# Kernel optimization log

Hardware: AMD Instinct MI355X
Metric: run time of the kernel (lower is better)

The kernel has to match this reference:

```python
import jax, jax.numpy as jnp
import numpy as np

N_STATE = 1024
N_HEAD = 16
HEAD_DIM = N_STATE // N_HEAD


def setup_inputs() -> dict:
    key = jax.random.key(0)
    ks = jax.random.split(key, 8)
    B, S = 8, 1500
    x = jax.random.normal(ks[0], (B, S, N_STATE), dtype=jnp.float32)
    # additive causal mask (0 on/below diagonal, -inf above), broadcast over B,H
    neg = jnp.float32(-1e9)
    mask = jnp.where(jnp.tril(jnp.ones((S, S), dtype=bool)), 0.0, neg).astype(jnp.float32)
    s = 0.02
    Wq = jax.random.normal(ks[1], (N_STATE, N_STATE), dtype=jnp.float32) * s
    bq = jnp.zeros((N_STATE,), dtype=jnp.float32)
    Wk = jax.random.normal(ks[2], (N_STATE, N_STATE), dtype=jnp.float32) * s
    Wv = jax.random.normal(ks[3], (N_STATE, N_STATE), dtype=jnp.float32) * s
    bv = jnp.zeros((N_STATE,), dtype=jnp.float32)
    Wo = jax.random.normal(ks[4], (N_STATE, N_STATE), dtype=jnp.float32) * s
    bo = jnp.zeros((N_STATE,), dtype=jnp.float32)
    return {"x": x, "mask": mask, "Wq": Wq, "bq": bq, "Wk": Wk, "Wv": Wv, "bv": bv, "Wo": Wo, "bo": bo}


def reference(x, mask, Wq, bq, Wk, Wv, bv, Wo, bo):
    B, S, _ = x.shape
    # linear projections (torch Linear: x @ W^T + b); W stored as [out, in]
    q = x @ Wq.T + bq
    k = x @ Wk.T
    v = x @ Wv.T + bv
    # [B, H, S, D]
    q = q.reshape(B, S, N_HEAD, HEAD_DIM).transpose(0, 2, 1, 3)
    k = k.reshape(B, S, N_HEAD, HEAD_DIM).transpose(0, 2, 1, 3)
    v = v.reshape(B, S, N_HEAD, HEAD_DIM).transpose(0, 2, 1, 3)
    scale = 1.0 / np.sqrt(HEAD_DIM).astype(np.float32)
    scores = jnp.einsum('bhqd,bhkd->bhqk', q, k) * scale + mask
    attn = jax.nn.softmax(scores, axis=-1)
    out = jnp.einsum('bhqk,bhkd->bhqd', attn, v)
    out = out.transpose(0, 2, 1, 3).reshape(B, S, N_STATE)
    return out @ Wo.T + bo
```

## Files before the change

kernel.cpp:

```cpp
#include <hip/hip_runtime.h>
#include <hip/hip_bf16.h>

#define N_STATE 1024
#define N_HEAD  16
#define D_HEAD  64
#define BATCH   8
#define SEQ     1500
#define ROWS    (BATCH*SEQ)
#define SVP     1536
#define MTILES  94

#define BM 128
#define BN 128
#define BK 32
#define BK2 64

typedef __bf16 bf16x8 __attribute__((ext_vector_type(8)));
typedef __bf16 bf16x4 __attribute__((ext_vector_type(4)));
typedef float  f32x4  __attribute__((ext_vector_type(4)));

__device__ __forceinline__ f32x4 mfma16(bf16x8 a, bf16x8 b, f32x4 c) {
  return __builtin_amdgcn_mfma_f32_16x16x32_bf16(a, b, c, 0, 0, 0);
}

__device__ __forceinline__ void gl_lds16(const void* g, void* l) {
  __builtin_amdgcn_global_load_lds(
      (const __attribute__((address_space(1))) unsigned int*)g,
      (__attribute__((address_space(3))) unsigned int*)l, 16, 0, 0);
}

__global__ __launch_bounds__(256)
void cvt_all(const float* __restrict__ x,  const float* __restrict__ wq,
             const float* __restrict__ wk, const float* __restrict__ wv,
             const float* __restrict__ wo,
             __bf16* __restrict__ xb, __bf16* __restrict__ wb)
{
  const int which = blockIdx.y;
  const float* src;
  __bf16* dst;
  size_t n;
  if (which == 0) { src = x; dst = xb; n = (size_t)ROWS * N_STATE; }
  else {
    src = (which == 1) ? wq : (which == 2) ? wk : (which == 3) ? wv : wo;
    dst = wb + (size_t)(which - 1) * N_STATE * N_STATE;
    n = (size_t)N_STATE * N_STATE;
  }
  const size_t stride = (size_t)gridDim.x * 256 * 4;
  for (size_t i = ((size_t)blockIdx.x * 256 + threadIdx.x) * 4; i < n; i += stride) {
    const f32x4 v = *(const f32x4*)(src + i);
    bf16x4 c; c[0]=(__bf16)v[0]; c[1]=(__bf16)v[1]; c[2]=(__bf16)v[2]; c[3]=(__bf16)v[3];
    *(bf16x4*)(dst + i) = c;
  }
}

__global__ __launch_bounds__(256)
void qkv_fast(const __bf16* __restrict__ xb, const __bf16* __restrict__ wb,
              const float* __restrict__ bq, const float* __restrict__ bv,
              __bf16* __restrict__ q_ws, __bf16* __restrict__ k_ws,
              __bf16* __restrict__ vt_ws)
{
  const int xcd = blockIdx.x & 7;
  const int jj  = blockIdx.x >> 3;
  const int nt  = jj & 7;
  const int mt  = (jj >> 3) * 8 + xcd;
  if (mt >= MTILES) return;

  __shared__ __bf16 lA[BM * BK2];
  __shared__ __bf16 lB[BN * BK2];
  const int which = blockIdx.z;
  const __bf16* W = wb + (size_t)which * N_STATE * N_STATE;

  const int tid = threadIdx.x;
  const int lane = tid & 63, wave = tid >> 6;
  const int l15 = lane & 15, quad = lane >> 4;
  const int wr = wave >> 1, wc = wave & 1;

  f32x4 acc[4][4] = {};

  for (int k0 = 0; k0 < N_STATE; k0 += BK2) {
#pragma unroll
    for (int t = 0; t < 4; ++t) {
      const int c = wave * 4 + t;
      const int s = c * 64 + lane;
      const int row = s >> 3;
      const int sw  = (lane & 7) ^ (row & 7);
      const int ga = min(mt * BM + row, ROWS - 1);
      gl_lds16(xb + (size_t)ga * N_STATE + k0 + sw * 8, (__bf16*)lA + c * 512);
      const int gb = nt * BN + row;
      gl_lds16(W + (size_t)gb * N_STATE + k0 + sw * 8, (__bf16*)lB + c * 512);
    }
    __syncthreads();
#pragma unroll
    for (int h = 0; h < 2; ++h) {
      bf16x8 af[4], bfr[4];
#pragma unroll
      for (int i = 0; i < 4; ++i) {
        const int ra = wr * 64 + i * 16 + l15;
        const int rb = wc * 64 + i * 16 + l15;
        af[i]  = *(const bf16x8*)&lA[ra * BK2 + (((h * 4 + quad) ^ (ra & 7)) * 8)];
        bfr[i] = *(const bf16x8*)&lB[rb * BK2 + (((h * 4 + quad) ^ (rb & 7)) * 8)];
      }
      if (which != 2) {
#pragma unroll
        for (int i = 0; i < 4; ++i)
#pragma unroll
          for (int j = 0; j < 4; ++j)
            acc[i][j] = mfma16(af[i], bfr[j], acc[i][j]);
      } else {
#pragma unroll
        for (int i = 0; i < 4; ++i)
#pragma unroll
          for (int j = 0; j < 4; ++j)
            acc[i][j] = mfma16(bfr[j], af[i], acc[i][j]);
      }
    }
    __syncthreads();
  }

  if (which != 2) {
#pragma unroll
    for (int i = 0; i < 4; ++i) {
      const int mrow = mt * BM + wr * 64 + i * 16 + quad * 4;
#pragma unroll
      for (int j = 0; j < 4; ++j) {
        const int col = nt * BN + wc * 64 + j * 16 + l15;
        const int h = col >> 6, d = col & 63;
        const float badd = (which == 0) ? bq[col] : 0.0f;
        __bf16* dst = (which == 0) ? q_ws : k_ws;
#pragma unroll
        for (int r = 0; r < 4; ++r) {
          const int row = mrow + r;
          if (row < ROWS) {
            const int b = row / SEQ, s = row % SEQ;
            dst[(((size_t)(b * N_HEAD + h)) * SEQ + s) * D_HEAD + d] =
                (__bf16)(acc[i][j][r] + badd);
          }
        }
      }
    }
  } else {
#pragma unroll
    for (int i = 0; i < 4; ++i) {
      const int sg = mt * BM + wr * 64 + i * 16 + l15;
      const bool valid = sg < ROWS;
      const int b = sg / SEQ, srow = sg % SEQ;
#pragma unroll
      for (int j = 0; j < 4; ++j) {
        const int dbase = nt * BN + wc * 64 + j * 16 + quad * 4;
#pragma unroll
        for (int r = 0; r < 4; ++r) {
          const int d = dbase + r;
          const int h = d >> 6, dd = d & 63;
          if (valid)
            vt_ws[(((size_t)(b * N_HEAD + h)) * D_HEAD + dd) * SVP + srow] =
                (__bf16)(acc[i][j][r] + bv[d]);
        }
      }
    }
  }
}

__global__ __launch_bounds__(256)
void out_fast(const __bf16* __restrict__ a_in, const __bf16* __restrict__ wob,
              const float* __restrict__ bo, float* __restrict__ out)
{
  const int xcd = blockIdx.x & 7;
  const int jj  = blockIdx.x >> 3;
  const int nt  = jj & 7;
  const int mt  = (jj >> 3) * 8 + xcd;
  if (mt >= MTILES) return;

  __shared__ __bf16 lA[BM * BK2];
  __shared__ __bf16 lB[BN * BK2];
  const int tid = threadIdx.x;
  const int lane = tid & 63, wave = tid >> 6;
  const int l15 = lane & 15, quad = lane >> 4;
  const int wr = wave >> 1, wc = wave & 1;

  f32x4 acc[4][4] = {};

  for (int k0 = 0; k0 < N_STATE; k0 += BK2) {
#pragma unroll
    for (int t = 0; t < 4; ++t) {
      const int c = wave * 4 + t;
      const int s = c * 64 + lane;
      const int row = s >> 3;
      const int sw  = (lane & 7) ^ (row & 7);
      const int ga = min(mt * BM + row, ROWS - 1);
      gl_lds16(a_in + (size_t)ga * N_STATE + k0 + sw * 8, (__bf16*)lA + c * 512);
      const int gb = nt * BN + row;
      gl_lds16(wob + (size_t)gb * N_STATE + k0 + sw * 8, (__bf16*)lB + c * 512);
    }
    __syncthreads();
#pragma unroll
    for (int h = 0; h < 2; ++h) {
      bf16x8 af[4], bfr[4];
#pragma unroll
      for (int i = 0; i < 4; ++i) {
        const int ra = wr * 64 + i * 16 + l15;
        const int rb = wc * 64 + i * 16 + l15;
        af[i]  = *(const bf16x8*)&lA[ra * BK2 + (((h * 4 + quad) ^ (ra & 7)) * 8)];
        bfr[i] = *(const bf16x8*)&lB[rb * BK2 + (((h * 4 + quad) ^ (rb & 7)) * 8)];
      }
#pragma unroll
      for (int i = 0; i < 4; ++i)
#pragma unroll
        for (int j = 0; j < 4; ++j)
          acc[i][j] = mfma16(af[i], bfr[j], acc[i][j]);
    }
    __syncthreads();
  }

#pragma unroll
  for (int i = 0; i < 4; ++i) {
    const int mrow = mt * BM + wr * 64 + i * 16 + quad * 4;
#pragma unroll
    for (int j = 0; j < 4; ++j) {
      const int col = nt * BN + wc * 64 + j * 16 + l15;
      const float badd = bo[col];
#pragma unroll
      for (int r = 0; r < 4; ++r) {
        const int row = mrow + r;
        if (row < ROWS)
          out[(size_t)row * N_STATE + col] = acc[i][j][r] + badd;
      }
    }
  }
}

__global__ __launch_bounds__(256)
void qkv_gemm(const float* __restrict__ x,
              const float* __restrict__ Wq, const float* __restrict__ bq,
              const float* __restrict__ Wk,
              const float* __restrict__ Wv, const float* __restrict__ bv,
              __bf16* __restrict__ q_ws, __bf16* __restrict__ k_ws,
              __bf16* __restrict__ vt_ws)
{
  __shared__ __bf16 lA[BM * BK];
  __shared__ __bf16 lB[BN * BK];
  const int which = blockIdx.z;
  const float* W    = (which == 0) ? Wq : (which == 1) ? Wk : Wv;
  const float* bias = (which == 0) ? bq : (which == 2) ? bv : nullptr;

  const int mt = blockIdx.x, nt = blockIdx.y;
  const int tid = threadIdx.x;
  const int lane = tid & 63, wave = tid >> 6;
  const int l15 = lane & 15, quad = lane >> 4;
  const int wr = wave >> 1, wc = wave & 1;

  f32x4 acc[4][4] = {};

  for (int k0 = 0; k0 < N_STATE; k0 += BK) {
#pragma unroll
    for (int it = 0; it < 4; ++it) {
      const int s = tid + it * 256;
      const int row = s >> 3, seg = s & 7;
      const int ga = min(mt * BM + row, ROWS - 1);
      const f32x4 va = *(const f32x4*)(x + (size_t)ga * N_STATE + k0 + seg * 4);
      bf16x4 ca; ca[0]=(__bf16)va[0]; ca[1]=(__bf16)va[1];
                 ca[2]=(__bf16)va[2]; ca[3]=(__bf16)va[3];
      *(bf16x4*)&lA[row * BK + seg * 4] = ca;
      const int gb = nt * BM + row;
      const f32x4 vb = *(const f32x4*)(W + (size_t)gb * N_STATE + k0 + seg * 4);
      bf16x4 cb; cb[0]=(__bf16)vb[0]; cb[1]=(__bf16)vb[1];
                 cb[2]=(__bf16)vb[2]; cb[3]=(__bf16)vb[3];
      *(bf16x4*)&lB[row * BK + seg * 4] = cb;
    }
    __syncthreads();
    bf16x8 af[4], bfr[4];
#pragma unroll
    for (int i = 0; i < 4; ++i) {
      af[i]  = *(const bf16x8*)&lA[(wr * 64 + i * 16 + l15) * BK + quad * 8];
      bfr[i] = *(const bf16x8*)&lB[(wc * 64 + i * 16 + l15) * BK + quad * 8];
    }
    if (which != 2) {
#pragma unroll
      for (int i = 0; i < 4; ++i)
#pragma unroll
        for (int j = 0; j < 4; ++j)
          acc[i][j] = mfma16(af[i], bfr[j], acc[i][j]);
    } else {
#pragma unroll
      for (int i = 0; i < 4; ++i)
#pragma unroll
        for (int j = 0; j < 4; ++j)
          acc[i][j] = mfma16(bfr[j], af[i], acc[i][j]);
    }
    __syncthreads();
  }

  if (which != 2) {
#pragma unroll
    for (int i = 0; i < 4; ++i) {
      const int mrow = mt * BM + wr * 64 + i * 16 + quad * 4;
#pragma unroll
      for (int j = 0; j < 4; ++j) {
        const int col = nt * BN + wc * 64 + j * 16 + l15;
        const int h = col >> 6, d = col & 63;
        const float badd = bias ? bias[col] : 0.0f;
        __bf16* dst = (which == 0) ? q_ws : k_ws;
#pragma unroll
        for (int r = 0; r < 4; ++r) {
          const int row = mrow + r;
          if (row < ROWS) {
            const int b = row / SEQ, s = row % SEQ;
            dst[(((size_t)(b * N_HEAD + h)) * SEQ + s) * D_HEAD + d] =
                (__bf16)(acc[i][j][r] + badd);
          }
        }
      }
    }
  } else {
#pragma unroll
    for (int i = 0; i < 4; ++i) {
      const int sg = mt * BM + wr * 64 + i * 16 + l15;
      const bool valid = sg < ROWS;
      const int b = sg / SEQ, srow = sg % SEQ;
#pragma unroll
      for (int j = 0; j < 4; ++j) {
        const int dbase = nt * BN + wc * 64 + j * 16 + quad * 4;
#pragma unroll
        for (int r = 0; r < 4; ++r) {
          const int d = dbase + r;
          const int h = d >> 6, dd = d & 63;
          if (valid)
            vt_ws[(((size_t)(b * N_HEAD + h)) * D_HEAD + dd) * SVP + srow] =
                (__bf16)(acc[i][j][r] + bias[d]);
        }
      }
    }
  }
}

__global__ __launch_bounds__(256)
void flash_attn(const __bf16* __restrict__ q_ws, const __bf16* __restrict__ k_ws,
                const __bf16* __restrict__ vt_ws, __bf16* __restrict__ attn)
{
  __shared__ __align__(16) __bf16 lK[8 * 512];
  __shared__ __align__(16) __bf16 lV[8 * 512];
  __shared__ __align__(16) __bf16 lP[4 * 16 * 72];
  const int bh = blockIdx.x;
  const int qt = gridDim.y - 1 - blockIdx.y;
  const int tid = threadIdx.x, lane = tid & 63, wave = tid >> 6;
  const int l15 = lane & 15, quad = lane >> 4;
  const __bf16* Q  = q_ws  + (size_t)bh * SEQ * D_HEAD;
  const __bf16* K  = k_ws  + (size_t)bh * SEQ * D_HEAD;
  const __bf16* Vt = vt_ws + (size_t)bh * D_HEAD * SVP;
  __bf16* lPw = lP + wave * 16 * 72;

  const int q0 = qt * 64, wq0 = q0 + wave * 16;
  const int qload = min(wq0 + l15, SEQ - 1);
  const bf16x8 qa0 = *(const bf16x8*)(Q + (size_t)qload * D_HEAD + quad * 8);
  const bf16x8 qa1 = *(const bf16x8*)(Q + (size_t)qload * D_HEAD + 32 + quad * 8);

  const float NEG = -1.0e30f;
  const float scale = 0.125f;
  const int query = wq0 + l15;
  f32x4 o[4] = {};
  float m_i = NEG, l_i = 0.0f;

  const int kmax = min(q0 + 63, SEQ - 1);
  const int wqmax = wq0 + 15;

  for (int kt = 0; kt <= kmax; kt += 64) {
#pragma unroll
    for (int t = 0; t < 2; ++t) {
      const int c = wave * 2 + t;
      const int gk = min(kt + lane, SEQ - 1);
      gl_lds16(K + (size_t)gk * D_HEAD + c * 8, (__bf16*)lK + c * 512);
      gl_lds16(Vt + (size_t)lane * SVP + kt + c * 8, (__bf16*)lV + c * 512);
    }
    __syncthreads();

    if (kt <= wqmax) {
      f32x4 sg[4] = {};
#pragma unroll
      for (int g = 0; g < 4; ++g) {
        const bf16x8 k0 = *(const bf16x8*)&lK[quad * 512 + (g * 16 + l15) * 8];
        const bf16x8 k1 = *(const bf16x8*)&lK[(4 + quad) * 512 + (g * 16 + l15) * 8];
        sg[g] = mfma16(k0, qa0, sg[g]);
        sg[g] = mfma16(k1, qa1, sg[g]);
      }
      const bool fullvis = (kt + 63 <= wq0) && (kt + 63 < SEQ);
      float tmax = NEG;
#pragma unroll
      for (int g = 0; g < 4; ++g)
#pragma unroll
        for (int r = 0; r < 4; ++r) {
          float v = sg[g][r] * scale;
          if (!fullvis) {
            const int key = kt + g * 16 + quad * 4 + r;
            v = (key <= query && key < SEQ) ? v : NEG;
          }
          sg[g][r] = v;
          tmax = fmaxf(tmax, v);
        }
      tmax = fmaxf(tmax, __shfl_xor(tmax, 16));
      tmax = fmaxf(tmax, __shfl_xor(tmax, 32));
      const float mnew = fmaxf(m_i, tmax);
      const float alpha = __expf(m_i - mnew);
      float rsum = 0.0f;
#pragma unroll
      for (int g = 0; g < 4; ++g) {
        bf16x4 pk;
#pragma unroll
        for (int r = 0; r < 4; ++r) {
          const float e = __expf(sg[g][r] - mnew);
          rsum += e;
          pk[r] = (__bf16)e;
        }
        *(bf16x4*)&lPw[l15 * 72 + g * 16 + quad * 4] = pk;
      }
      rsum += __shfl_xor(rsum, 16);
      rsum += __shfl_xor(rsum, 32);
      l_i = l_i * alpha + rsum;
      m_i = mnew;
#pragma unroll
      for (int nn = 0; nn < 4; ++nn)
#pragma unroll
        for (int r = 0; r < 4; ++r) o[nn][r] *= alpha;

#pragma unroll
      for (int h = 0; h < 2; ++h) {
        const bf16x8 pb = *(const bf16x8*)&lPw[l15 * 72 + h * 32 + quad * 8];
#pragma unroll
        for (int nn = 0; nn < 4; ++nn) {
          const bf16x8 va =
              *(const bf16x8*)&lV[(h * 4 + quad) * 512 + (nn * 16 + l15) * 8];
          o[nn] = mfma16(va, pb, o[nn]);
        }
      }
    }
    __syncthreads();
  }

  const int b = bh >> 4, hh = bh & 15;
  if (query < SEQ) {
    const float inv = 1.0f / l_i;
#pragma unroll
    for (int nn = 0; nn < 4; ++nn) {
      bf16x4 ov;
#pragma unroll
      for (int r = 0; r < 4; ++r) ov[r] = (__bf16)(o[nn][r] * inv);
      *(bf16x4*)&attn[(((size_t)(b * SEQ + query)) * N_HEAD + hh) * D_HEAD +
                      nn * 16 + quad * 4] = ov;
    }
  }
}

__global__ __launch_bounds__(256)
void out_gemm(const __bf16* __restrict__ a_in, const float* __restrict__ Wo,
              const float* __restrict__ bo, float* __restrict__ out)
{
  __shared__ __bf16 lA[BM * BK];
  __shared__ __bf16 lB[BN * BK];
  const int mt = blockIdx.x, nt = blockIdx.y;
  const int tid = threadIdx.x;
  const int lane = tid & 63, wave = tid >> 6;
  const int l15 = lane & 15, quad = lane >> 4;
  const int wr = wave >> 1, wc = wave & 1;

  f32x4 acc[4][4] = {};

  for (int k0 = 0; k0 < N_STATE; k0 += BK) {
#pragma unroll
    for (int it = 0; it < 2; ++it) {
      const int s = tid + it * 256;
      const int row = s >> 2, seg = s & 3;
      const int ga = min(mt * BM + row, ROWS - 1);
      *(bf16x8*)&lA[row * BK + seg * 8] =
          *(const bf16x8*)(a_in + (size_t)ga * N_STATE + k0 + seg * 8);
    }
#pragma unroll
    for (int it = 0; it < 4; ++it) {
      const int s = tid + it * 256;
      const int row = s >> 3, seg = s & 7;
      const int gb = nt * BM + row;
      const f32x4 vb = *(const f32x4*)(Wo + (size_t)gb * N_STATE + k0 + seg * 4);
      bf16x4 cb; cb[0]=(__bf16)vb[0]; cb[1]=(__bf16)vb[1];
                 cb[2]=(__bf16)vb[2]; cb[3]=(__bf16)vb[3];
      *(bf16x4*)&lB[row * BK + seg * 4] = cb;
    }
    __syncthreads();
    bf16x8 af[4], bfr[4];
#pragma unroll
    for (int i = 0; i < 4; ++i) {
      af[i]  = *(const bf16x8*)&lA[(wr * 64 + i * 16 + l15) * BK + quad * 8];
      bfr[i] = *(const bf16x8*)&lB[(wc * 64 + i * 16 + l15) * BK + quad * 8];
    }
#pragma unroll
    for (int i = 0; i < 4; ++i)
#pragma unroll
      for (int j = 0; j < 4; ++j)
        acc[i][j] = mfma16(af[i], bfr[j], acc[i][j]);
    __syncthreads();
  }

#pragma unroll
  for (int i = 0; i < 4; ++i) {
    const int mrow = mt * BM + wr * 64 + i * 16 + quad * 4;
#pragma unroll
    for (int j = 0; j < 4; ++j) {
      const int col = nt * BN + wc * 64 + j * 16 + l15;
      const float badd = bo[col];
#pragma unroll
      for (int r = 0; r < 4; ++r) {
        const int row = mrow + r;
        if (row < ROWS)
          out[(size_t)row * N_STATE + col] = acc[i][j][r] + badd;
      }
    }
  }
}

extern "C" void kernel_launch(void* const* d_in, const int* in_sizes, int n_in,
                              void* d_out, int out_size, void* d_ws, size_t ws_size,
                              hipStream_t stream) {
  const float* x  = (const float*)d_in[0];
  const float* Wq = (const float*)d_in[2];
  const float* bq = (const float*)d_in[3];
  const float* Wk = (const float*)d_in[4];
  const float* Wv = (const float*)d_in[5];
  const float* bv = (const float*)d_in[6];
  const float* Wo = (const float*)d_in[7];
  const float* bo = (const float*)d_in[8];
  float* out = (float*)d_out;

  const size_t chunk  = (size_t)ROWS * N_STATE;
  const size_t vchunk = (size_t)BATCH * N_HEAD * D_HEAD * SVP;
  const size_t wchunk = (size_t)4 * N_STATE * N_STATE;
  __bf16* q_ws  = (__bf16*)d_ws;
  __bf16* k_ws  = q_ws + chunk;
  __bf16* vt_ws = k_ws + chunk;
  __bf16* attn  = vt_ws + vchunk;
  __bf16* xb    = attn;
  __bf16* wb    = attn + chunk;
  const size_t need = (3 * chunk + vchunk + wchunk) * sizeof(__bf16);

  const int MT = (ROWS + BM - 1) / BM;
  if (ws_size >= need) {
    cvt_all<<<dim3(1024, 5), 256, 0, stream>>>(x, Wq, Wk, Wv, Wo, xb, wb);
    qkv_fast<<<dim3(768, 1, 3), 256, 0, stream>>>(
        xb, wb, bq, bv, q_ws, k_ws, vt_ws);
    flash_attn<<<dim3(BATCH * N_HEAD, (SEQ + 63) / 64), 256, 0, stream>>>(
        q_ws, k_ws, vt_ws, attn);
    out_fast<<<dim3(768, 1, 1), 256, 0, stream>>>(
        attn, wb + (size_t)3 * N_STATE * N_STATE, bo, out);
  } else {
    qkv_gemm<<<dim3(MT, N_STATE / BN, 3), 256, 0, stream>>>(
        x, Wq, bq, Wk, Wv, bv, q_ws, k_ws, vt_ws);
    flash_attn<<<dim3(BATCH * N_HEAD, (SEQ + 63) / 64), 256, 0, stream>>>(
        q_ws, k_ws, vt_ws, attn);
    out_gemm<<<dim3(MT, N_STATE / BN), 256, 0, stream>>>(attn, Wo, bo, out);
  }
}
```

Baseline: 382.3 us.

## Double-buffer LDS tiles and use 8 waves per block in projection GEMMs

The QKV and output projection GEMMs now keep two LDS buffers. The next K-tile is loaded asynchronously with global_load_lds while the current tile is consumed, and a partial vmcnt wait stands in for the full barrier before each compute step. Each block grows from 4 to 8 waves, each wave computing a 64x32 sub-tile, so per-wave accumulators halve and occupancy hints are added. The aim is to hide global-memory latency behind MFMA work, at the cost of twice the LDS per block, which may limit how many blocks fit per CU.

```diff
diff --git a/kernel.cpp b/kernel.cpp
--- a/kernel.cpp
+++ b/kernel.cpp
@@ -27,6 +27,13 @@
   __builtin_amdgcn_global_load_lds(
       (const __attribute__((address_space(1))) unsigned int*)g,
       (__attribute__((address_space(3))) unsigned int*)l, 16, 0, 0);
+}
+
+__device__ __forceinline__ void bar() {
+  __builtin_amdgcn_sched_barrier(0);
+  __builtin_amdgcn_s_barrier();
+  __builtin_amdgcn_sched_barrier(0);
+  asm volatile("" ::: "memory");
 }
 
 __global__ __launch_bounds__(256)
@@ -53,11 +60,11 @@
   }
 }
 
-__global__ __launch_bounds__(256)
-void qkv_fast(const __bf16* __restrict__ xb, const __bf16* __restrict__ wb,
-              const float* __restrict__ bq, const float* __restrict__ bv,
-              __bf16* __restrict__ q_ws, __bf16* __restrict__ k_ws,
-              __bf16* __restrict__ vt_ws)
+__global__ __launch_bounds__(512, 4)
+void qkv_db(const __bf16* __restrict__ xb, const __bf16* __restrict__ wb,
+            const float* __restrict__ bq, const float* __restrict__ bv,
+            __bf16* __restrict__ q_ws, __bf16* __restrict__ k_ws,
+            __bf16* __restrict__ vt_ws)
 {
   const int xcd = blockIdx.x & 7;
   const int jj  = blockIdx.x >> 3;
@@ -65,56 +72,74 @@
   const int mt  = (jj >> 3) * 8 + xcd;
   if (mt >= MTILES) return;
 
-  __shared__ __bf16 lA[BM * BK2];
-  __shared__ __bf16 lB[BN * BK2];
+  __shared__ __bf16 lA[2][BM * BK2];
+  __shared__ __bf16 lB[2][BN * BK2];
   const int which = blockIdx.z;
   const __bf16* W = wb + (size_t)which * N_STATE * N_STATE;
 
   const int tid = threadIdx.x;
   const int lane = tid & 63, wave = tid >> 6;
   const int l15 = lane & 15, quad = lane >> 4;
-  const int wr = wave >> 1, wc = wave & 1;
-
-  f32x4 acc[4][4] = {};
-
-  for (int k0 = 0; k0 < N_STATE; k0 += BK2) {
-#pragma unroll
-    for (int t = 0; t < 4; ++t) {
-      const int c = wave * 4 + t;
+  const int wr = wave & 1, wc = wave >> 1;
+
+  f32x4 acc[4][2] = {};
+
+  auto stage = [&](int kt) {
+    const int k0 = kt * BK2;
+    __bf16* dA = (__bf16*)lA[kt & 1];
+    __bf16* dB = (__bf16*)lB[kt & 1];
+#pragma unroll
+    for (int t = 0; t < 2; ++t) {
+      const int c = wave * 2 + t;
       const int s = c * 64 + lane;
       const int row = s >> 3;
       const int sw  = (lane & 7) ^ (row & 7);
       const int ga = min(mt * BM + row, ROWS - 1);
-      gl_lds16(xb + (size_t)ga * N_STATE + k0 + sw * 8, (__bf16*)lA + c * 512);
+      gl_lds16(xb + (size_t)ga * N_STATE + k0 + sw * 8, dA + c * 512);
       const int gb = nt * BN + row;
-      gl_lds16(W + (size_t)gb * N_STATE + k0 + sw * 8, (__bf16*)lB + c * 512);
-    }
-    __syncthreads();
+      gl_lds16(W + (size_t)gb * N_STATE + k0 + sw * 8, dB + c * 512);
+    }
+  };
+
+  stage(0);
+  for (int kt = 0; kt < N_STATE / BK2; ++kt) {
+    if (kt < N_STATE / BK2 - 1) {
+      stage(kt + 1);
+      asm volatile("s_waitcnt vmcnt(4)" ::: "memory");
+    } else {
+      asm volatile("s_waitcnt vmcnt(0)" ::: "memory");
+    }
+    bar();
+    const __bf16* cA = lA[kt & 1];
+    const __bf16* cB = lB[kt & 1];
 #pragma unroll
     for (int h = 0; h < 2; ++h) {
-      bf16x8 af[4], bfr[4];
+      bf16x8 af[4], bfr[2];
 #pragma unroll
       for (int i = 0; i < 4; ++i) {
         const int ra = wr * 64 + i * 16 + l15;
-        const int rb = wc * 64 + i * 16 + l15;
-        af[i]  = *(const bf16x8*)&lA[ra * BK2 + (((h * 4 + quad) ^ (ra & 7)) * 8)];
-        bfr[i] = *(const bf16x8*)&lB[rb * BK2 + (((h * 4 + quad) ^ (rb & 7)) * 8)];
+        af[i] = *(const bf16x8*)&cA[ra * BK2 + (((h * 4 + quad) ^ (ra & 7)) * 8)];
+      }
+#pragma unroll
+      for (int j = 0; j < 2; ++j) {
+        const int rb = wc * 32 + j * 16 + l15;
+        bfr[j] = *(const bf16x8*)&cB[rb * BK2 + (((h * 4 + quad) ^ (rb & 7)) * 8)];
       }
       if (which != 2) {
 #pragma unroll
         for (int i = 0; i < 4; ++i)
 #pragma unroll
-          for (int j = 0; j < 4; ++j)
+          for (int j = 0; j < 2; ++j)
             acc[i][j] = mfma16(af[i], bfr[j], acc[i][j]);
       } else {
 #pragma unroll
         for (int i = 0; i < 4; ++i)
 #pragma unroll
-          for (int j = 0; j < 4; ++j)
+          for (int j = 0; j < 2; ++j)
             acc[i][j] = mfma16(bfr[j], af[i], acc[i][j]);
       }
     }
-    __syncthreads();
+    bar();
   }
 
   if (which != 2) {
@@ -122,8 +147,8 @@
     for (int i = 0; i < 4; ++i) {
       const int mrow = mt * BM + wr * 64 + i * 16 + quad * 4;
 #pragma unroll
-      for (int j = 0; j < 4; ++j) {
-        const int col = nt * BN + wc * 64 + j * 16 + l15;
+      for (int j = 0; j < 2; ++j) {
+        const int col = nt * BN + wc * 32 + j * 16 + l15;
         const int h = col >> 6, d = col & 63;
         const float badd = (which == 0) ? bq[col] : 0.0f;
         __bf16* dst = (which == 0) ? q_ws : k_ws;
@@ -145,8 +170,8 @@
       const bool valid = sg < ROWS;
       const int b = sg / SEQ, srow = sg % SEQ;
 #pragma unroll
-      for (int j = 0; j < 4; ++j) {
-        const int dbase = nt * BN + wc * 64 + j * 16 + quad * 4;
+      for (int j = 0; j < 2; ++j) {
+        const int dbase = nt * BN + wc * 32 + j * 16 + quad * 4;
 #pragma unroll
         for (int r = 0; r < 4; ++r) {
           const int d = dbase + r;
@@ -160,9 +185,9 @@
   }
 }
 
-__global__ __launch_bounds__(256)
-void out_fast(const __bf16* __restrict__ a_in, const __bf16* __restrict__ wob,
-              const float* __restrict__ bo, float* __restrict__ out)
+__global__ __launch_bounds__(512, 4)
+void out_db(const __bf16* __restrict__ a_in, const __bf16* __restrict__ wob,
+            const float* __restrict__ bo, float* __restrict__ out)
 {
   const int xcd = blockIdx.x & 7;
   const int jj  = blockIdx.x >> 3;
@@ -170,53 +195,71 @@
   const int mt  = (jj >> 3) * 8 + xcd;
   if (mt >= MTILES) return;
 
-  __shared__ __bf16 lA[BM * BK2];
-  __shared__ __bf16 lB[BN * BK2];
+  __shared__ __bf16 lA[2][BM * BK2];
+  __shared__ __bf16 lB[2][BN * BK2];
   const int tid = threadIdx.x;
   const int lane = tid & 63, wave = tid >> 6;
   const int l15 = lane & 15, quad = lane >> 4;
-  const int wr = wave >> 1, wc = wave & 1;
-
-  f32x4 acc[4][4] = {};
-
-  for (int k0 = 0; k0 < N_STATE; k0 += BK2) {
-#pragma unroll
-    for (int t = 0; t < 4; ++t) {
-      const int c = wave * 4 + t;
+  const int wr = wave & 1, wc = wave >> 1;
+
+  f32x4 acc[4][2] = {};
+
+  auto stage = [&](int kt) {
+    const int k0 = kt * BK2;
+    __bf16* dA = (__bf16*)lA[kt & 1];
+    __bf16* dB = (__bf16*)lB[kt & 1];
+#pragma unroll
+    for (int t = 0; t < 2; ++t) {
+      const int c = wave * 2 + t;
       const int s = c * 64 + lane;
       const int row = s >> 3;
       const int sw  = (lane & 7) ^ (row & 7);
       const int ga = min(mt * BM + row, ROWS - 1);
-      gl_lds16(a_in + (size_t)ga * N_STATE + k0 + sw * 8, (__bf16*)lA + c * 512);
+      gl_lds16(a_in + (size_t)ga * N_STATE + k0 + sw * 8, dA + c * 512);
       const int gb = nt * BN + row;
-      gl_lds16(wob + (size_t)gb * N_STATE + k0 + sw * 8, (__bf16*)lB + c * 512);
-    }
-    __syncthreads();
+      gl_lds16(wob + (size_t)gb * N_STATE + k0 + sw * 8, dB + c * 512);
+    }
+  };
+
+  stage(0);
+  for (int kt = 0; kt < N_STATE / BK2; ++kt) {
+    if (kt < N_STATE / BK2 - 1) {
+      stage(kt + 1);
+      asm volatile("s_waitcnt vmcnt(4)" ::: "memory");
+    } else {
+      asm volatile("s_waitcnt vmcnt(0)" ::: "memory");
+    }
+    bar();
+    const __bf16* cA = lA[kt & 1];
+    const __bf16* cB = lB[kt & 1];
 #pragma unroll
     for (int h = 0; h < 2; ++h) {
-      bf16x8 af[4], bfr[4];
+      bf16x8 af[4], bfr[2];
 #pragma unroll
       for (int i = 0; i < 4; ++i) {
         const int ra = wr * 64 + i * 16 + l15;
-        const int rb = wc * 64 + i * 16 + l15;
-        af[i]  = *(const bf16x8*)&lA[ra * BK2 + (((h * 4 + quad) ^ (ra & 7)) * 8)];
-        bfr[i] = *(const bf16x8*)&lB[rb * BK2 + (((h * 4 + quad) ^ (rb & 7)) * 8)];
+        af[i] = *(const bf16x8*)&cA[ra * BK2 + (((h * 4 + quad) ^ (ra & 7)) * 8)];
+      }
+#pragma unroll
+      for (int j = 0; j < 2; ++j) {
+        const int rb = wc * 32 + j * 16 + l15;
+        bfr[j] = *(const bf16x8*)&cB[rb * BK2 + (((h * 4 + quad) ^ (rb & 7)) * 8)];
       }
 #pragma unroll
       for (int i = 0; i < 4; ++i)
 #pragma unroll
-        for (int j = 0; j < 4; ++j)
+        for (int j = 0; j < 2; ++j)
           acc[i][j] = mfma16(af[i], bfr[j], acc[i][j]);
     }
-    __syncthreads();
+    bar();
   }
 
 #pragma unroll
   for (int i = 0; i < 4; ++i) {
     const int mrow = mt * BM + wr * 64 + i * 16 + quad * 4;
 #pragma unroll
-    for (int j = 0; j < 4; ++j) {
-      const int col = nt * BN + wc * 64 + j * 16 + l15;
+    for (int j = 0; j < 2; ++j) {
+      const int col = nt * BN + wc * 32 + j * 16 + l15;
       const float badd = bo[col];
 #pragma unroll
       for (int r = 0; r < 4; ++r) {
@@ -540,11 +583,11 @@
   const int MT = (ROWS + BM - 1) / BM;
   if (ws_size >= need) {
     cvt_all<<<dim3(1024, 5), 256, 0, stream>>>(x, Wq, Wk, Wv, Wo, xb, wb);
-    qkv_fast<<<dim3(768, 1, 3), 256, 0, stream>>>(
+    qkv_db<<<dim3(768, 1, 3), 512, 0, stream>>>(
         xb, wb, bq, bv, q_ws, k_ws, vt_ws);
     flash_attn<<<dim3(BATCH * N_HEAD, (SEQ + 63) / 64), 256, 0, stream>>>(
         q_ws, k_ws, vt_ws, attn);
-    out_fast<<<dim3(768, 1, 1), 256, 0, stream>>>(
+    out_db<<<dim3(768, 1, 1), 512, 0, stream>>>(
         attn, wb + (size_t)3 * N_STATE * N_STATE, bo, out);
   } else {
     qkv_gemm<<<dim3(MT, N_STATE / BN, 3), 256, 0, stream>>>(
```

Result: faster. 351.7 us (-8.0%).
